# Kernel tuning notes

Hardware: AMD Instinct MI355X
Metric: run time of the kernel (lower is better)

Reference implementation:

```python
import jax, jax.numpy as jnp
import numpy as np

L, H, D, HD, FF, V, S, B = 2, 16, 1024, 64, 4096, 32000, 1024, 4
SCALE = jnp.sqrt(jnp.float32(HD))
EPS = 1e-5


def _ln(x, w, b):
    m = jnp.mean(x, axis=-1, keepdims=True)
    v = jnp.var(x, axis=-1, keepdims=True)
    return (x - m) / jnp.sqrt(v + EPS) * w + b


def setup_inputs() -> dict:
    key = jax.random.key(0)
    ks = jax.random.split(key, 12)
    std = 0.02
    inp = {
        "x": jax.random.randint(ks[0], (B, S), 0, V, dtype=jnp.int64),
        "tok_emb": jax.random.normal(ks[1], (V, D), jnp.float32) * std,
        "pos_emb": jax.random.normal(ks[2], (S, D), jnp.float32) * std,
        "Wq": jax.random.normal(ks[3], (L, H, D, HD), jnp.float32) * std,
        "bq": jnp.zeros((L, H, HD), jnp.float32),
        "Wk": jax.random.normal(ks[4], (L, H, D, HD), jnp.float32) * std,
        "bk": jnp.zeros((L, H, HD), jnp.float32),
        "Wv": jax.random.normal(ks[5], (L, H, D, HD), jnp.float32) * std,
        "bv": jnp.zeros((L, H, HD), jnp.float32),
        "Wo": jax.random.normal(ks[6], (L, D, D), jnp.float32) * std,
        "bo": jnp.zeros((L, D), jnp.float32),
        "ln1_w": jnp.ones((L, D), jnp.float32),
        "ln1_b": jnp.zeros((L, D), jnp.float32),
        "ln2_w": jnp.ones((L, D), jnp.float32),
        "ln2_b": jnp.zeros((L, D), jnp.float32),
        "W1": jax.random.normal(ks[7], (L, D, FF), jnp.float32) * std,
        "b1": jnp.zeros((L, FF), jnp.float32),
        "W2": jax.random.normal(ks[8], (L, FF, D), jnp.float32) * std,
        "b2": jnp.zeros((L, D), jnp.float32),
        "Wout": jax.random.normal(ks[9], (D, V), jnp.float32) * std,
        "bout": jnp.zeros((V,), jnp.float32),
    }
    return inp


def reference(x, tok_emb, pos_emb, Wq, bq, Wk, bk, Wv, bv, Wo, bo,
              ln1_w, ln1_b, ln2_w, ln2_b, W1, b1, W2, b2, Wout, bout):
    Bsz, Slen = x.shape
    h = tok_emb[x] + pos_emb[None, :Slen, :]  # [B,S,D]
    mask = jnp.tril(jnp.ones((Slen, Slen), dtype=bool))  # causal
    for l in range(L):
        # all heads batched: per-head wq/wk/wv (dim -> head_dim each)
        q = jnp.einsum('bsd,hde->bhse', h, Wq[l]) + bq[l][None, :, None, :]
        k = jnp.einsum('bsd,hde->bhse', h, Wk[l]) + bk[l][None, :, None, :]
        v = jnp.einsum('bsd,hde->bhse', h, Wv[l]) + bv[l][None, :, None, :]
        att = jnp.einsum('bhqe,bhke->bhqk', q, k) / SCALE
        att = jnp.where(mask[None, None], att, -jnp.inf)
        att = jax.nn.softmax(att, axis=-1)
        o = jnp.einsum('bhqk,bhke->bhqe', att, v)
        o = o.transpose(0, 2, 1, 3).reshape(Bsz, Slen, D)  # concat heads
        o = o @ Wo[l] + bo[l]
        h = _ln(h + o, ln1_w[l], ln1_b[l])
        f = jax.nn.gelu(h @ W1[l] + b1[l], approximate=False) @ W2[l] + b2[l]
        h = _ln(h + f, ln2_w[l], ln2_b[l])
    logits = h @ Wout + bout
    return logits, h
```

## Files before the change

kernel.cpp:

```cpp
#include <hip/hip_runtime.h>
#include <stdint.h>

#define S_LEN  1024
#define DMODEL 1024
#define NH     16
#define HD     64
#define FFDIM  4096
#define VOCAB  32000
#define BATCH  4
#define LAYERS 2
#define MTOT   (BATCH * S_LEN)

typedef __bf16 bf16x8 __attribute__((ext_vector_type(8)));
typedef float  f32x4  __attribute__((ext_vector_type(4)));
typedef unsigned short ushort8v __attribute__((ext_vector_type(8)));
typedef unsigned short ushort4v __attribute__((ext_vector_type(4)));
typedef unsigned short u16;

__device__ __forceinline__ u16 f2bf(float f) {
  union { float f; uint32_t u; } c; c.f = f;
  uint32_t u = c.u;
  u += 0x7FFFu + ((u >> 16) & 1u);
  return (u16)(u >> 16);
}

__device__ __forceinline__ f32x4 fzero4() {
  f32x4 z; z[0] = 0.f; z[1] = 0.f; z[2] = 0.f; z[3] = 0.f; return z;
}

#define GLD16(gp, lp)                                                                  \
  __builtin_amdgcn_global_load_lds(                                                    \
      (const __attribute__((address_space(1))) unsigned int*)(gp),                     \
      (__attribute__((address_space(3))) unsigned int*)(lp), 16, 0, 0)

__global__ __launch_bounds__(256) void transpose_cvt(const float* __restrict__ in,
                                                     u16* __restrict__ out,
                                                     int R, int C) {
  const int64_t boff = (int64_t)blockIdx.z * R * C;
  in += boff; out += boff;
  const int r0 = blockIdx.y * 64, c0 = blockIdx.x * 64;
  __shared__ float tile[64][65];
  const int t = threadIdx.x;
#pragma unroll
  for (int p = 0; p < 4; ++p) {
    int r = p * 16 + (t >> 4);
    int c = (t & 15) * 4;
    float4 v = *(const float4*)(in + (int64_t)(r0 + r) * C + c0 + c);
    tile[r][c] = v.x; tile[r][c + 1] = v.y; tile[r][c + 2] = v.z; tile[r][c + 3] = v.w;
  }
  __syncthreads();
#pragma unroll
  for (int p = 0; p < 4; ++p) {
    int c = p * 16 + (t >> 4);
    int rg = (t & 15) * 4;
    ushort4v o;
    o[0] = f2bf(tile[rg][c]);     o[1] = f2bf(tile[rg + 1][c]);
    o[2] = f2bf(tile[rg + 2][c]); o[3] = f2bf(tile[rg + 3][c]);
    *(ushort4v*)(out + (int64_t)(c0 + c) * R + r0 + rg) = o;
  }
}

__global__ __launch_bounds__(256) void embed_kernel(const int* __restrict__ x,
                                                    const float* __restrict__ tok,
                                                    const float* __restrict__ pos,
                                                    float* __restrict__ resid,
                                                    u16* __restrict__ hbf) {
  const int row = blockIdx.x;
  const int s = row & (S_LEN - 1);
  const int c = threadIdx.x * 4;
  const int id = x[row];
  const float4 tv = *(const float4*)(tok + (int64_t)id * DMODEL + c);
  const float4 pv = *(const float4*)(pos + (int64_t)s * DMODEL + c);
  float4 v; v.x = tv.x + pv.x; v.y = tv.y + pv.y; v.z = tv.z + pv.z; v.w = tv.w + pv.w;
  *(float4*)(resid + (int64_t)row * DMODEL + c) = v;
  ushort4v o; o[0] = f2bf(v.x); o[1] = f2bf(v.y); o[2] = f2bf(v.z); o[3] = f2bf(v.w);
  *(ushort4v*)(hbf + (int64_t)row * DMODEL + c) = o;
}

__global__ __launch_bounds__(256) void ln_kernel(const float* __restrict__ xin,
                                                 const float* __restrict__ w,
                                                 const float* __restrict__ bb,
                                                 float* __restrict__ fout,
                                                 u16* __restrict__ bout) {
  const int row = blockIdx.x;
  const int t = threadIdx.x;
  const int c = t * 4;
  const float4 v = *(const float4*)(xin + (int64_t)row * DMODEL + c);
  float s = v.x + v.y + v.z + v.w;
  float sq = v.x * v.x + v.y * v.y + v.z * v.z + v.w * v.w;
#pragma unroll
  for (int off = 1; off < 64; off <<= 1) {
    s += __shfl_xor(s, off);
    sq += __shfl_xor(sq, off);
  }
  __shared__ float red[8];
  if ((t & 63) == 0) { red[t >> 6] = s; red[4 + (t >> 6)] = sq; }
  __syncthreads();
  s = red[0] + red[1] + red[2] + red[3];
  sq = red[4] + red[5] + red[6] + red[7];
  const float mean = s * (1.0f / 1024.0f);
  const float var = sq * (1.0f / 1024.0f) - mean * mean;
  const float rstd = rsqrtf(var + 1e-5f);
  const float4 w4 = *(const float4*)(w + c);
  const float4 b4 = *(const float4*)(bb + c);
  float o0 = (v.x - mean) * rstd * w4.x + b4.x;
  float o1 = (v.y - mean) * rstd * w4.y + b4.y;
  float o2 = (v.z - mean) * rstd * w4.z + b4.z;
  float o3 = (v.w - mean) * rstd * w4.w + b4.w;
  float4 ov; ov.x = o0; ov.y = o1; ov.z = o2; ov.w = o3;
  *(float4*)(fout + (int64_t)row * DMODEL + c) = ov;
  ushort4v ob; ob[0] = f2bf(o0); ob[1] = f2bf(o1); ob[2] = f2bf(o2); ob[3] = f2bf(o3);
  *(ushort4v*)(bout + (int64_t)row * DMODEL + c) = ob;
}

__device__ __forceinline__ void gemm_core(const u16* __restrict__ A,
                                          const u16* __restrict__ Bt,
                                          int K, int64_t m0, int64_t n0,
                                          u16* As, u16* Bs, f32x4 acc[4][4]) {
  const int t = threadIdx.x;
  const int lane = t & 63;
  const int g = lane >> 4, ln = lane & 15;
  const int wv = t >> 6;
  const int wm = (wv & 1) * 64, wn = (wv >> 1) * 64;

  const u16* ga0 = A + (m0 + (t >> 2)) * (int64_t)K + (t & 3) * 8;
  const u16* ga1 = ga0 + (int64_t)64 * K;
  const u16* gb0 = Bt + (n0 + (t >> 2)) * (int64_t)K + (t & 3) * 8;
  const u16* gb1 = gb0 + (int64_t)64 * K;
  u16* la0 = As + t * 8;
  u16* la1 = As + 2048 + t * 8;
  u16* lb0 = Bs + t * 8;
  u16* lb1 = Bs + 2048 + t * 8;

  const int nk = K >> 5;
  for (int kt = 0; kt < nk; ++kt) {
    if (kt) __syncthreads();
    GLD16(ga0, la0); GLD16(ga1, la1);
    GLD16(gb0, lb0); GLD16(gb1, lb1);
    ga0 += 32; ga1 += 32; gb0 += 32; gb1 += 32;
    __syncthreads();
    bf16x8 af[4], bfr[4];
#pragma unroll
    for (int i = 0; i < 4; ++i)
      af[i] = *(const bf16x8*)(As + (wm + i * 16 + ln) * 32 + g * 8);
#pragma unroll
    for (int j = 0; j < 4; ++j)
      bfr[j] = *(const bf16x8*)(Bs + (wn + j * 16 + ln) * 32 + g * 8);
#pragma unroll
    for (int i = 0; i < 4; ++i)
#pragma unroll
      for (int j = 0; j < 4; ++j)
        acc[i][j] = __builtin_amdgcn_mfma_f32_16x16x32_bf16(af[i], bfr[j], acc[i][j], 0, 0, 0);
  }
}

template <int MODE>
__device__ __forceinline__ void gemm_epi(f32x4 acc[4][4], const float* __restrict__ bias,
                                         const float* __restrict__ resid,
                                         float* __restrict__ outf, u16* __restrict__ outb,
                                         int64_t m0, int64_t n0, int N) {
  const int t = threadIdx.x;
  const int lane = t & 63, wv = t >> 6;
  const int g = lane >> 4, ln = lane & 15;
  const int64_t wmb = m0 + (wv & 1) * 64;
  const int64_t wnb = n0 + (wv >> 1) * 64;
#pragma unroll
  for (int j = 0; j < 4; ++j) {
    const int64_t col = wnb + j * 16 + ln;
    const float bj = bias[col];
#pragma unroll
    for (int i = 0; i < 4; ++i) {
#pragma unroll
      for (int r = 0; r < 4; ++r) {
        const int64_t row = wmb + i * 16 + g * 4 + r;
        const int64_t idx = row * (int64_t)N + col;
        float v = acc[i][j][r] + bj;
        if (MODE == 1) v = 0.5f * v * (1.0f + erff(v * 0.70710678118f));
        if (MODE == 2) v += resid[idx];
        if (MODE <= 1) outb[idx] = f2bf(v);
        else           outf[idx] = v;
      }
    }
  }
}

template <int MODE, int REMAP>
__global__ __launch_bounds__(256) void gemm_kernel(const u16* __restrict__ A,
                                                   const u16* __restrict__ Bt,
                                                   const float* __restrict__ bias,
                                                   const float* __restrict__ resid,
                                                   float* __restrict__ outf,
                                                   u16* __restrict__ outb,
                                                   int K, int N) {
  __shared__ u16 As[4096];
  __shared__ u16 Bs[4096];
  f32x4 acc[4][4];
#pragma unroll
  for (int i = 0; i < 4; ++i)
#pragma unroll
    for (int j = 0; j < 4; ++j) acc[i][j] = fzero4();
  int bxi = blockIdx.x, byi = blockIdx.y;
  if (REMAP) {
    const int lid = byi * 250 + bxi;
    const int chunk = lid / 800;
    const int within = lid - chunk * 800;
    const int w2 = (within & 7) * 100 + (within >> 3);
    byi = w2 & 31;
    bxi = chunk * 25 + (w2 >> 5);
  }
  const int64_t m0 = (int64_t)byi * 128;
  const int64_t n0 = (int64_t)bxi * 128;
  gemm_core(A, Bt, K, m0, n0, As, Bs, acc);
  gemm_epi<MODE>(acc, bias, resid, outf, outb, m0, n0, N);
}

__global__ __launch_bounds__(256) void gemm_qkv_kernel(const u16* __restrict__ A,
    const u16* __restrict__ btq, const u16* __restrict__ btk, const u16* __restrict__ btv,
    const float* __restrict__ bq, const float* __restrict__ bk, const float* __restrict__ bv,
    u16* __restrict__ oq, u16* __restrict__ ok, u16* __restrict__ ov) {
  const int z = blockIdx.z;
  const u16* Bt = (z == 0) ? btq : (z == 1) ? btk : btv;
  const float* bias = (z == 0) ? bq : (z == 1) ? bk : bv;
  u16* ob = (z == 0) ? oq : (z == 1) ? ok : ov;
  __shared__ u16 As[4096];
  __shared__ u16 Bs[4096];
  f32x4 acc[4][4];
#pragma unroll
  for (int i = 0; i < 4; ++i)
#pragma unroll
    for (int j = 0; j < 4; ++j) acc[i][j] = fzero4();
  const int64_t m0 = (int64_t)blockIdx.y * 128;
  const int64_t n0 = (int64_t)blockIdx.x * 128;
  gemm_core(A, Bt, DMODEL, m0, n0, As, Bs, acc);
  gemm_epi<0>(acc, bias, nullptr, nullptr, ob, m0, n0, DMODEL);
}

__global__ __launch_bounds__(256) void transpose_v_kernel(const u16* __restrict__ vb,
                                                          u16* __restrict__ vt) {
  const int bh = blockIdx.y;
  const int b = bh >> 4, h = bh & 15;
  const int s0 = blockIdx.x * 64;
  const int t = threadIdx.x;
  __shared__ u16 tile[64][80];
#pragma unroll
  for (int p = 0; p < 2; ++p) {
    int sr = p * 32 + (t >> 3);
    int c = (t & 7) * 8;
    ushort8v v = *(const ushort8v*)(vb + ((int64_t)(b * S_LEN + s0 + sr)) * DMODEL + h * HD + c);
    *(ushort8v*)(&tile[sr][c]) = v;
  }
  __syncthreads();
#pragma unroll
  for (int p = 0; p < 2; ++p) {
    int d = p * 32 + (t >> 3);
    int sg = (t & 7) * 8;
    ushort8v o;
#pragma unroll
    for (int j = 0; j < 8; ++j) o[j] = tile[sg + j][d];
    *(ushort8v*)(vt + ((int64_t)(bh * HD + d)) * S_LEN + s0 + sg) = o;
  }
}

__global__ __launch_bounds__(256) void attn_kernel(const u16* __restrict__ qb,
                                                   const u16* __restrict__ kb,
                                                   const u16* __restrict__ vt,
                                                   u16* __restrict__ ob) {
  const int qblk = blockIdx.x, h = blockIdx.y, b = blockIdx.z;
  const int t = threadIdx.x;
  const int wv = t >> 6, lane = t & 63;
  const int g = lane >> 4, ln = lane & 15;
  __shared__ u16 Ks[32 * 64];
  __shared__ u16 Vts[64 * 32];
  __shared__ u16 Ps[4][16 * 40];
  const int q0 = qblk * 64;

  const u16* qptr = qb + ((int64_t)(b * S_LEN + q0 + wv * 16 + ln)) * DMODEL + h * HD;
  const bf16x8 qf0 = *(const bf16x8*)(qptr + g * 8);
  const bf16x8 qf1 = *(const bf16x8*)(qptr + 32 + g * 8);

  f32x4 oo[4];
  float m_i[4], l_i[4];
#pragma unroll
  for (int r = 0; r < 4; ++r) { oo[r] = fzero4(); m_i[r] = -1e30f; l_i[r] = 0.f; }

  const int ntiles = (q0 >> 5) + 2;
  const u16* kbase = kb + ((int64_t)(b * S_LEN)) * DMODEL + h * HD;
  const u16* vbase = vt + ((int64_t)((b * NH + h) * HD)) * S_LEN;

  for (int kt = 0; kt < ntiles; ++kt) {
    const int k0 = kt * 32;
    if (kt) __syncthreads();
    GLD16(kbase + (int64_t)(k0 + (t >> 3)) * DMODEL + (t & 7) * 8, &Ks[t * 8]);
    GLD16(vbase + (int64_t)(t >> 2) * S_LEN + k0 + (t & 3) * 8, &Vts[t * 8]);
    __syncthreads();

    f32x4 s0 = fzero4(), s1 = fzero4();
    {
      bf16x8 ka = *(const bf16x8*)(&Ks[ln * 64 + g * 8]);
      bf16x8 kbf = *(const bf16x8*)(&Ks[ln * 64 + 32 + g * 8]);
      s0 = __builtin_amdgcn_mfma_f32_16x16x32_bf16(qf0, ka, s0, 0, 0, 0);
      s0 = __builtin_amdgcn_mfma_f32_16x16x32_bf16(qf1, kbf, s0, 0, 0, 0);
      bf16x8 kc = *(const bf16x8*)(&Ks[(16 + ln) * 64 + g * 8]);
      bf16x8 kd = *(const bf16x8*)(&Ks[(16 + ln) * 64 + 32 + g * 8]);
      s1 = __builtin_amdgcn_mfma_f32_16x16x32_bf16(qf0, kc, s1, 0, 0, 0);
      s1 = __builtin_amdgcn_mfma_f32_16x16x32_bf16(qf1, kd, s1, 0, 0, 0);
    }
#pragma unroll
    for (int r = 0; r < 4; ++r) {
      const int qg = q0 + wv * 16 + g * 4 + r;
      float sc0 = s0[r] * 0.125f;
      float sc1 = s1[r] * 0.125f;
      if (k0 + ln > qg)      sc0 = -1e30f;
      if (k0 + 16 + ln > qg) sc1 = -1e30f;
      float mx = fmaxf(sc0, sc1);
#pragma unroll
      for (int off = 1; off < 16; off <<= 1) mx = fmaxf(mx, __shfl_xor(mx, off));
      const float mnew = fmaxf(m_i[r], mx);
      const float p0 = __expf(sc0 - mnew);
      const float p1 = __expf(sc1 - mnew);
      float rs = p0 + p1;
#pragma unroll
      for (int off = 1; off < 16; off <<= 1) rs += __shfl_xor(rs, off);
      const float alpha = __expf(m_i[r] - mnew);
      l_i[r] = l_i[r] * alpha + rs;
      m_i[r] = mnew;
      oo[0][r] *= alpha; oo[1][r] *= alpha; oo[2][r] *= alpha; oo[3][r] *= alpha;
      Ps[wv][(g * 4 + r) * 40 + ln] = f2bf(p0);
      Ps[wv][(g * 4 + r) * 40 + 16 + ln] = f2bf(p1);
    }
    __threadfence_block();
    const bf16x8 pf = *(const bf16x8*)(&Ps[wv][ln * 40 + g * 8]);
#pragma unroll
    for (int j = 0; j < 4; ++j) {
      bf16x8 vf = *(const bf16x8*)(&Vts[(j * 16 + ln) * 32 + g * 8]);
      oo[j] = __builtin_amdgcn_mfma_f32_16x16x32_bf16(pf, vf, oo[j], 0, 0, 0);
    }
  }
#pragma unroll
  for (int r = 0; r < 4; ++r) {
    const float inv = 1.0f / l_i[r];
    const int64_t row = (int64_t)(b * S_LEN + q0 + wv * 16 + g * 4 + r);
#pragma unroll
    for (int j = 0; j < 4; ++j)
      ob[row * DMODEL + h * HD + j * 16 + ln] = f2bf(oo[j][r] * inv);
  }
}

extern "C" void kernel_launch(void* const* d_in, const int* in_sizes, int n_in,
                              void* d_out, int out_size, void* d_ws, size_t ws_size,
                              hipStream_t stream) {
  const int*   x    = (const int*)d_in[0];
  const float* tok  = (const float*)d_in[1];
  const float* pos  = (const float*)d_in[2];
  const float* Wq   = (const float*)d_in[3];
  const float* bq   = (const float*)d_in[4];
  const float* Wk   = (const float*)d_in[5];
  const float* bk   = (const float*)d_in[6];
  const float* Wv   = (const float*)d_in[7];
  const float* bv   = (const float*)d_in[8];
  const float* Wo   = (const float*)d_in[9];
  const float* bo   = (const float*)d_in[10];
  const float* ln1w = (const float*)d_in[11];
  const float* ln1b = (const float*)d_in[12];
  const float* ln2w = (const float*)d_in[13];
  const float* ln2b = (const float*)d_in[14];
  const float* W1   = (const float*)d_in[15];
  const float* b1   = (const float*)d_in[16];
  const float* W2   = (const float*)d_in[17];
  const float* b2   = (const float*)d_in[18];
  const float* Wout = (const float*)d_in[19];
  const float* bout = (const float*)d_in[20];

  float* outF = (float*)d_out;
  float* hOut = outF + (int64_t)MTOT * VOCAB;

  char* ws = (char*)d_ws;
  int64_t off = 0;
  auto carve = [&](int64_t bytes) { char* p = ws + off; off += (bytes + 255) & ~255LL; return p; };
  u16* wqT   = (u16*)carve((int64_t)LAYERS * DMODEL * DMODEL * 2);
  u16* wkT   = (u16*)carve((int64_t)LAYERS * DMODEL * DMODEL * 2);
  u16* wvT   = (u16*)carve((int64_t)LAYERS * DMODEL * DMODEL * 2);
  u16* woT   = (u16*)carve((int64_t)LAYERS * DMODEL * DMODEL * 2);
  u16* w1T   = (u16*)carve((int64_t)LAYERS * FFDIM * DMODEL * 2);
  u16* w2T   = (u16*)carve((int64_t)LAYERS * DMODEL * FFDIM * 2);
  u16* woutT = (u16*)carve((int64_t)VOCAB * DMODEL * 2);
  u16* hbf   = (u16*)carve((int64_t)MTOT * DMODEL * 2);
  u16* qbuf  = (u16*)carve((int64_t)MTOT * DMODEL * 2);
  u16* kbuf  = (u16*)carve((int64_t)MTOT * DMODEL * 2);
  u16* vbuf  = (u16*)carve((int64_t)MTOT * DMODEL * 2);
  u16* vtb   = (u16*)carve((int64_t)MTOT * DMODEL * 2);
  u16* abuf  = (u16*)carve((int64_t)MTOT * DMODEL * 2);
  u16* ffb   = (u16*)carve((int64_t)MTOT * FFDIM * 2);
  float* resid = (float*)carve((int64_t)MTOT * DMODEL * 4);
  float* x1    = (float*)carve((int64_t)MTOT * DMODEL * 4);

  const dim3 blk(256);

  transpose_cvt<<<dim3(1, 16, LAYERS * NH), blk, 0, stream>>>(Wq, wqT, DMODEL, HD);
  transpose_cvt<<<dim3(1, 16, LAYERS * NH), blk, 0, stream>>>(Wk, wkT, DMODEL, HD);
  transpose_cvt<<<dim3(1, 16, LAYERS * NH), blk, 0, stream>>>(Wv, wvT, DMODEL, HD);
  transpose_cvt<<<dim3(16, 16, LAYERS), blk, 0, stream>>>(Wo, woT, DMODEL, DMODEL);
  transpose_cvt<<<dim3(64, 16, LAYERS), blk, 0, stream>>>(W1, w1T, DMODEL, FFDIM);
  transpose_cvt<<<dim3(16, 64, LAYERS), blk, 0, stream>>>(W2, w2T, FFDIM, DMODEL);
  transpose_cvt<<<dim3(500, 16, 1), blk, 0, stream>>>(Wout, woutT, DMODEL, VOCAB);

  embed_kernel<<<MTOT, blk, 0, stream>>>(x, tok, pos, resid, hbf);

  for (int l = 0; l < LAYERS; ++l) {
    const int64_t wOff  = (int64_t)l * DMODEL * DMODEL;
    const int64_t w1Off = (int64_t)l * FFDIM * DMODEL;
    gemm_qkv_kernel<<<dim3(8, 32, 3), blk, 0, stream>>>(
        hbf, wqT + wOff, wkT + wOff, wvT + wOff,
        bq + l * DMODEL, bk + l * DMODEL, bv + l * DMODEL, qbuf, kbuf, vbuf);
    transpose_v_kernel<<<dim3(16, 64), blk, 0, stream>>>(vbuf, vtb);
    attn_kernel<<<dim3(16, 16, 4), blk, 0, stream>>>(qbuf, kbuf, vtb, abuf);
    gemm_kernel<2, 0><<<dim3(8, 32), blk, 0, stream>>>(
        abuf, woT + wOff, bo + l * DMODEL, resid, x1, nullptr, DMODEL, DMODEL);
    ln_kernel<<<MTOT, blk, 0, stream>>>(x1, ln1w + l * DMODEL, ln1b + l * DMODEL, resid, hbf);
    gemm_kernel<1, 0><<<dim3(32, 32), blk, 0, stream>>>(
        hbf, w1T + w1Off, b1 + l * FFDIM, nullptr, nullptr, ffb, DMODEL, FFDIM);
    gemm_kernel<2, 0><<<dim3(8, 32), blk, 0, stream>>>(
        ffb, w2T + w1Off, b2 + l * DMODEL, resid, x1, nullptr, FFDIM, DMODEL);
    float* lnout = (l == LAYERS - 1) ? hOut : resid;
    ln_kernel<<<MTOT, blk, 0, stream>>>(x1, ln2w + l * DMODEL, ln2b + l * DMODEL, lnout, hbf);
  }

  gemm_kernel<3, 1><<<dim3(250, 32), blk, 0, stream>>>(
      hbf, woutT, bout, nullptr, outF, nullptr, DMODEL, VOCAB);
}
```

Measured before the change: 1.860 ms.

## Triple-buffer GEMM shared-memory tiles with async prefetch two stages ahead

Replaces the single-buffered GEMM k-loop, which had two barriers per step and exposed global-to-LDS load latency, with a three-stage ring buffer. Loads for tile kt+2 are issued before computing tile kt, and a partial vmcnt wait plus a single barrier gates each step. This should hide load latency behind MFMA work. In exchange LDS use per block triples to 48KB, which may cut occupancy.

Measured after the change: 1.904 ms. 1.02x slower.

```diff
diff --git a/kernel.cpp b/kernel.cpp
--- a/kernel.cpp
+++ b/kernel.cpp
@@ -32,6 +32,13 @@
   __builtin_amdgcn_global_load_lds(                                                    \
       (const __attribute__((address_space(1))) unsigned int*)(gp),                     \
       (__attribute__((address_space(3))) unsigned int*)(lp), 16, 0, 0)
+
+#define WAITBAR(N)                                                                     \
+  do {                                                                                 \
+    asm volatile("s_waitcnt vmcnt(" #N ")" ::: "memory");                              \
+    __builtin_amdgcn_sched_barrier(0);                                                 \
+    __builtin_amdgcn_s_barrier();                                                      \
+  } while (0)
 
 __global__ __launch_bounds__(256) void transpose_cvt(const float* __restrict__ in,
                                                      u16* __restrict__ out,
@@ -127,30 +134,45 @@
   const u16* ga1 = ga0 + (int64_t)64 * K;
   const u16* gb0 = Bt + (n0 + (t >> 2)) * (int64_t)K + (t & 3) * 8;
   const u16* gb1 = gb0 + (int64_t)64 * K;
-  u16* la0 = As + t * 8;
-  u16* la1 = As + 2048 + t * 8;
-  u16* lb0 = Bs + t * 8;
-  u16* lb1 = Bs + 2048 + t * 8;
+  const int to8 = t * 8;
 
   const int nk = K >> 5;
+
+  GLD16(ga0, As + to8);              GLD16(ga1, As + 2048 + to8);
+  GLD16(gb0, Bs + to8);              GLD16(gb1, Bs + 2048 + to8);
+  GLD16(ga0 + 32, As + 4096 + to8);  GLD16(ga1 + 32, As + 4096 + 2048 + to8);
+  GLD16(gb0 + 32, Bs + 4096 + to8);  GLD16(gb1 + 32, Bs + 4096 + 2048 + to8);
+  WAITBAR(4);
+
+  int cur = 0;
   for (int kt = 0; kt < nk; ++kt) {
-    if (kt) __syncthreads();
-    GLD16(ga0, la0); GLD16(ga1, la1);
-    GLD16(gb0, lb0); GLD16(gb1, lb1);
-    ga0 += 32; ga1 += 32; gb0 += 32; gb1 += 32;
-    __syncthreads();
+    if (kt + 2 < nk) {
+      int st = cur + 2; if (st >= 3) st -= 3;
+      const int64_t goff = (int64_t)(kt + 2) * 32;
+      u16* da = As + st * 4096;
+      u16* db = Bs + st * 4096;
+      GLD16(ga0 + goff, da + to8);        GLD16(ga1 + goff, da + 2048 + to8);
+      GLD16(gb0 + goff, db + to8);        GLD16(gb1 + goff, db + 2048 + to8);
+    }
+    const u16* Ab = As + cur * 4096;
+    const u16* Bb = Bs + cur * 4096;
     bf16x8 af[4], bfr[4];
 #pragma unroll
     for (int i = 0; i < 4; ++i)
-      af[i] = *(const bf16x8*)(As + (wm + i * 16 + ln) * 32 + g * 8);
+      af[i] = *(const bf16x8*)(Ab + (wm + i * 16 + ln) * 32 + g * 8);
 #pragma unroll
     for (int j = 0; j < 4; ++j)
-      bfr[j] = *(const bf16x8*)(Bs + (wn + j * 16 + ln) * 32 + g * 8);
+      bfr[j] = *(const bf16x8*)(Bb + (wn + j * 16 + ln) * 32 + g * 8);
 #pragma unroll
     for (int i = 0; i < 4; ++i)
 #pragma unroll
       for (int j = 0; j < 4; ++j)
         acc[i][j] = __builtin_amdgcn_mfma_f32_16x16x32_bf16(af[i], bfr[j], acc[i][j], 0, 0, 0);
+    if (kt + 1 < nk) {
+      if (kt + 2 < nk) WAITBAR(4);
+      else             WAITBAR(0);
+    }
+    cur = cur + 1; if (cur >= 3) cur -= 3;
   }
 }
 
@@ -192,8 +214,8 @@
                                                    float* __restrict__ outf,
                                                    u16* __restrict__ outb,
                                                    int K, int N) {
-  __shared__ u16 As[4096];
-  __shared__ u16 Bs[4096];
+  __shared__ u16 As[3 * 4096];
+  __shared__ u16 Bs[3 * 4096];
   f32x4 acc[4][4];
 #pragma unroll
   for (int i = 0; i < 4; ++i)
@@ -222,8 +244,8 @@
   const u16* Bt = (z == 0) ? btq : (z == 1) ? btk : btv;
   const float* bias = (z == 0) ? bq : (z == 1) ? bk : bv;
   u16* ob = (z == 0) ? oq : (z == 1) ? ok : ov;
-  __shared__ u16 As[4096];
-  __shared__ u16 Bs[4096];
+  __shared__ u16 As[3 * 4096];
+  __shared__ u16 Bs[3 * 4096];
   f32x4 acc[4][4];
 #pragma unroll
   for (int i = 0; i < 4; ++i)
```
